# Kernel optimization log

Measured on AMD Instinct MI355X. Metric: run time of the kernel, lower is better.

Reference implementation:

```python
import jax, jax.numpy as jnp
import numpy as np

B, T, C = 2, 2048, 2048
H = 16
D = C // H  # 128 head dim
EPS = 1.1920929e-07  # torch RMSNorm default eps for fp32 (finfo.eps)
ROPE_BASE = 1000000.0


def setup_inputs() -> dict:
    key = jax.random.key(0)
    k1, k2, k3 = jax.random.split(key, 3)
    x = jax.random.normal(k1, (B, T, C), dtype=jnp.float32)
    w_qkv = jax.random.normal(k2, (C, 3 * C), dtype=jnp.float32) * (C ** -0.5)
    w_proj = jax.random.normal(k3, (C, C), dtype=jnp.float32) * (C ** -0.5)
    q_norm_w = jnp.ones((D,), dtype=jnp.float32)
    k_norm_w = jnp.ones((D,), dtype=jnp.float32)
    return {"x": x, "w_qkv": w_qkv, "w_proj": w_proj,
            "q_norm_w": q_norm_w, "k_norm_w": k_norm_w}


def _rms_norm(x, w):
    var = jnp.mean(jnp.square(x), axis=-1, keepdims=True)
    return x * jax.lax.rsqrt(var + EPS) * w


def _rope_tables(t_len, d_head, dtype):
    inv_freq = 1.0 / (ROPE_BASE ** (jnp.arange(0, d_head, 2, dtype=jnp.float32) / d_head))
    t = jnp.arange(t_len, dtype=jnp.float32)
    freqs = jnp.einsum('i,j->ij', t, inv_freq)          # [T, D/2]
    emb = jnp.concatenate([freqs, freqs], axis=-1)      # [T, D]
    return jnp.cos(emb).astype(dtype), jnp.sin(emb).astype(dtype)


def _rotate_half(x):
    x1, x2 = x[..., : x.shape[-1] // 2], x[..., x.shape[-1] // 2:]
    return jnp.concatenate([-x2, x1], axis=-1)


def reference(x, w_qkv, w_proj, q_norm_w, k_norm_w):
    b, t, c = x.shape
    qkv = x @ w_qkv                                     # [B, T, 3C]
    q, k, v = jnp.split(qkv, 3, axis=-1)
    # [B, H, T, D]
    q = q.reshape(b, t, H, D).transpose(0, 2, 1, 3)
    k = k.reshape(b, t, H, D).transpose(0, 2, 1, 3)
    v = v.reshape(b, t, H, D).transpose(0, 2, 1, 3)
    q = _rms_norm(q, q_norm_w)
    k = _rms_norm(k, k_norm_w)
    cos, sin = _rope_tables(t, D, x.dtype)              # [T, D]
    q = q * cos + _rotate_half(q) * sin
    k = k * cos + _rotate_half(k) * sin
    # NOTE: module uses scale = 1/d_head, not 1/sqrt(d_head)
    scale = 1.0 / D
    att = jnp.einsum('bhqd,bhkd->bhqk', q, k) * scale   # [B, H, T, T]
    causal = jnp.tril(jnp.ones((t, t), dtype=bool))
    att = jnp.where(causal, att, jnp.finfo(att.dtype).min)
    att = jax.nn.softmax(att, axis=-1)
    y = jnp.einsum('bhqk,bhkd->bhqd', att, v)           # [B, H, T, D]
    y = y.transpose(0, 2, 1, 3).reshape(b, t, c)
    return y @ w_proj
```

## Files before the change

### kernel.cpp

```cpp
#include <hip/hip_runtime.h>
#include <stdint.h>

#define Bb   2
#define Tt   2048
#define Cc_  2048
#define Hh   16
#define Dd   128
#define Mm_  4096
#define N1   6144
#define EPSf 1.1920929e-07f
#define SCALE (1.0f/128.0f)

typedef __bf16 bf16;
typedef __attribute__((ext_vector_type(8))) __bf16 bf16x8;
typedef __attribute__((ext_vector_type(4))) float  f32x4;

__device__ __forceinline__ void gl_lds16(const bf16* g, bf16* l) {
  __builtin_amdgcn_global_load_lds(
      (const __attribute__((address_space(1))) unsigned int*)g,
      (__attribute__((address_space(3))) unsigned int*)l, 16, 0, 0);
}

__global__ __launch_bounds__(256) void cvt_bf16(const float* __restrict__ in,
                                                bf16* __restrict__ out, int n) {
  int i = (blockIdx.x * 256 + threadIdx.x) * 4;
  if (i >= n) return;
  float4 v = *(const float4*)(in + i);
  union { bf16 h[4]; uint2 u; } o;
  o.h[0] = (bf16)v.x; o.h[1] = (bf16)v.y; o.h[2] = (bf16)v.z; o.h[3] = (bf16)v.w;
  *(uint2*)(out + i) = o.u;
}

__global__ __launch_bounds__(256) void transpose_cvt(const float* __restrict__ in,
                                                     bf16* __restrict__ out,
                                                     int R, int Cc) {
  __shared__ float tile[64][65];
  int c0 = blockIdx.x * 64, r0 = blockIdx.y * 64;
  int tid = threadIdx.x;
#pragma unroll
  for (int j = 0; j < 16; ++j) {
    int idx = tid + j * 256;
    int r = idx >> 6, c = idx & 63;
    tile[r][c] = in[(size_t)(r0 + r) * Cc + c0 + c];
  }
  __syncthreads();
#pragma unroll
  for (int j = 0; j < 16; ++j) {
    int idx = tid + j * 256;
    int rr = idx & 63, cc = idx >> 6;
    out[(size_t)(c0 + cc) * R + r0 + rr] = (bf16)tile[rr][cc];
  }
}

__global__ __launch_bounds__(256) void gemm_qkv_fused(
    const bf16* __restrict__ A, const bf16* __restrict__ Bt,
    const float* __restrict__ qw, const float* __restrict__ kw,
    bf16* __restrict__ Qg, bf16* __restrict__ Kg, bf16* __restrict__ VgT) {
  __shared__ __align__(16) bf16 smem[128 * 129];
  bf16* As = smem;
  bf16* Bs = smem + 128 * 64;
  const int Kk = Cc_;
  const int tid = threadIdx.x;
  const int wave = tid >> 6, lane = tid & 63;
  const int quad = lane >> 4, li = lane & 15;
  const int wm = wave >> 1, wn = wave & 1;
  const int m0 = blockIdx.y * 128, n0 = blockIdx.x * 128;

  f32x4 acc[4][4] = {};

  for (int kt = 0; kt < Kk; kt += 64) {
    __syncthreads();
#pragma unroll
    for (int j = 0; j < 4; ++j) {
      int c = j * 256 + tid;
      int r = c >> 3, cc = c & 7;
      int gc = ((cc ^ (r & 7)) << 3);
      gl_lds16(A + (size_t)(m0 + r) * Kk + kt + gc, &As[c * 8]);
      gl_lds16(Bt + (size_t)(n0 + r) * Kk + kt + gc, &Bs[c * 8]);
    }
    __syncthreads();
#pragma unroll
    for (int kc = 0; kc < 2; ++kc) {
      bf16x8 af[4], bfr[4];
#pragma unroll
      for (int t = 0; t < 4; ++t) {
        int rowa = wm * 64 + t * 16 + li;
        af[t] = *(const bf16x8*)&As[rowa * 64 + (((kc * 4 + quad) ^ (rowa & 7)) << 3)];
        int rowb = wn * 64 + t * 16 + li;
        bfr[t] = *(const bf16x8*)&Bs[rowb * 64 + (((kc * 4 + quad) ^ (rowb & 7)) << 3)];
      }
#pragma unroll
      for (int mi = 0; mi < 4; ++mi)
#pragma unroll
        for (int ni = 0; ni < 4; ++ni)
          acc[mi][ni] = __builtin_amdgcn_mfma_f32_16x16x32_bf16(af[mi], bfr[ni],
                                                                acc[mi][ni], 0, 0, 0);
    }
  }

  __syncthreads();
  bf16 (*tile)[129] = (bf16(*)[129])smem;
#pragma unroll
  for (int mi = 0; mi < 4; ++mi) {
    int row = wm * 64 + mi * 16 + quad * 4;
#pragma unroll
    for (int ni = 0; ni < 4; ++ni) {
      int col = wn * 64 + ni * 16 + li;
#pragma unroll
      for (int r = 0; r < 4; ++r)
        tile[row + r][col] = (bf16)acc[mi][ni][r];
    }
  }
  __syncthreads();

  const int s = blockIdx.x;
  const int b = m0 >> 11;
  const int tloc = m0 & 2047;

  if (s < 32) {
    const float* w = (s < 16) ? qw : kw;
    bf16* Og = (s < 16) ? Qg : Kg;
    const int h = s & 15;
    const float w1 = w[lane], w2 = w[lane + 64];
    const float invf = exp2f((float)lane * (-19.9315685693241740f / 64.0f));
    const size_t hb = (size_t)(b * Hh + h) * Tt;
    for (int rr = 0; rr < 32; ++rr) {
      int row = wave * 32 + rr;
      float x1 = (float)tile[row][lane], x2 = (float)tile[row][lane + 64];
      float ss = x1 * x1 + x2 * x2;
#pragma unroll
      for (int o = 1; o < 64; o <<= 1) ss += __shfl_xor(ss, o);
      float rn = rsqrtf(ss * (1.0f / 128.0f) + EPSf);
      x1 *= rn * w1; x2 *= rn * w2;
      int t = tloc + row;
      float sn, cs;
      sincosf((float)t * invf, &sn, &cs);
      size_t o1 = (hb + t) * Dd + lane;
      Og[o1]      = (bf16)(x1 * cs - x2 * sn);
      Og[o1 + 64] = (bf16)(x2 * cs + x1 * sn);
    }
  } else {
    const int h = s - 32;
    const size_t hb = (size_t)(b * Hh + h) * Dd;
#pragma unroll
    for (int it = 0; it < 8; ++it) {
      int d = it * 16 + (tid >> 4);
      int t0 = (tid & 15) * 8;
      bf16x8 v;
#pragma unroll
      for (int j = 0; j < 8; ++j) v[j] = tile[t0 + j][d];
      *(bf16x8*)(VgT + (hb + d) * Tt + tloc + t0) = v;
    }
  }
}

template <typename OutT>
__global__ __launch_bounds__(512, 2) void gemm256(const bf16* __restrict__ A,
                                                  const bf16* __restrict__ Bt,
                                                  OutT* __restrict__ Cm,
                                                  int Nn, int Kk) {
  __shared__ __align__(16) bf16 As[2][256 * 64];
  __shared__ __align__(16) bf16 Bs[2][128 * 64];
  const int tid = threadIdx.x;
  const int wave = tid >> 6, lane = tid & 63;
  const int quad = lane >> 4, li = lane & 15;
  const int wm = wave >> 2, wn = wave & 3;

  const int nwg = gridDim.x * gridDim.y;
  const int wg  = blockIdx.y * gridDim.x + blockIdx.x;
  const int swz = (wg & 7) * (nwg >> 3) + (wg >> 3);
  const int m0 = (swz / gridDim.x) * 256;
  const int n0 = (swz % gridDim.x) * 128;

  const int NT = Kk >> 6;
  const int lrow = lane >> 3;
  const int lchk = (lane & 7) ^ lrow;

  auto stageA = [&](int tt, int h, int cb) {
    int kt = (tt < NT ? tt : NT - 1) << 6;
#pragma unroll
    for (int j = 0; j < 2; ++j) {
      int seg = j * 8 + wave;
      int r0 = ((seg >> 3) << 7) + (h << 6) + ((seg & 7) << 3);
      gl_lds16(A + (size_t)(m0 + r0 + lrow) * Kk + kt + (lchk << 3),
               &As[cb][r0 * 64]);
    }
  };
  auto stageB = [&](int tt, int cb) {
    int kt = (tt < NT ? tt : NT - 1) << 6;
#pragma unroll
    for (int j = 0; j < 2; ++j) {
      int seg = j * 8 + wave;
      int r0 = seg << 3;
      gl_lds16(Bt + (size_t)(n0 + r0 + lrow) * Kk + kt + (lchk << 3),
               &Bs[cb][r0 * 64]);
    }
  };

  f32x4 acc[8][2] = {};
  bf16x8 afr[4][2], bfr[2][2];

  auto rdA = [&](int h, int cb) {
#pragma unroll
    for (int mi = 0; mi < 4; ++mi) {
      int r = wm * 128 + h * 64 + mi * 16 + li;
#pragma unroll
      for (int kc = 0; kc < 2; ++kc)
        afr[mi][kc] = *(const bf16x8*)&As[cb][r * 64 + (((kc * 4 + quad) ^ (r & 7)) << 3)];
    }
  };
  auto rdB = [&](int cb) {
#pragma unroll
    for (int nj = 0; nj < 2; ++nj) {
      int r = wn * 32 + nj * 16 + li;
#pragma unroll
      for (int kc = 0; kc < 2; ++kc)
        bfr[nj][kc] = *(const bf16x8*)&Bs[cb][r * 64 + (((kc * 4 + quad) ^ (r & 7)) << 3)];
    }
  };
  auto mmac = [&](int mo) {
    __builtin_amdgcn_s_setprio(1);
#pragma unroll
    for (int kc = 0; kc < 2; ++kc)
#pragma unroll
      for (int mi = 0; mi < 4; ++mi)
#pragma unroll
        for (int nj = 0; nj < 2; ++nj)
          acc[mo + mi][nj] = __builtin_amdgcn_mfma_f32_16x16x32_bf16(
              afr[mi][kc], bfr[nj][kc], acc[mo + mi][nj], 0, 0, 0);
    __builtin_amdgcn_s_setprio(0);
  };

  auto tile = [&](int t, int cur, int nxt) {
    rdA(0, cur); rdB(cur);
    stageA(t + 1, 1, nxt);
    asm volatile("s_waitcnt lgkmcnt(8)" ::: "memory");
    __builtin_amdgcn_s_barrier();
    asm volatile("s_waitcnt lgkmcnt(0)" ::: "memory");
    __builtin_amdgcn_sched_barrier(0);
    mmac(0);
    asm volatile("s_waitcnt vmcnt(6)" ::: "memory");
    __builtin_amdgcn_s_barrier();
    rdA(1, cur);
    stageA(t + 2, 0, cur);
    stageB(t + 2, cur);
    __builtin_amdgcn_s_barrier();
    asm volatile("s_waitcnt lgkmcnt(0)" ::: "memory");
    __builtin_amdgcn_sched_barrier(0);
    mmac(4);
    asm volatile("s_waitcnt vmcnt(6)" ::: "memory");
    __builtin_amdgcn_s_barrier();
  };

  stageA(0, 0, 0); stageB(0, 0); stageA(0, 1, 0);
  stageA(1, 0, 1); stageB(1, 1);
  asm volatile("s_waitcnt vmcnt(6)" ::: "memory");
  __builtin_amdgcn_s_barrier();

  for (int t = 0; t < NT; t += 2) {
    tile(t, 0, 1);
    tile(t + 1, 1, 0);
  }
  asm volatile("s_waitcnt vmcnt(0)" ::: "memory");

#pragma unroll
  for (int mi = 0; mi < 8; ++mi) {
    int row = m0 + wm * 128 + mi * 16 + quad * 4;
#pragma unroll
    for (int nj = 0; nj < 2; ++nj) {
      int col = n0 + wn * 32 + nj * 16 + li;
#pragma unroll
      for (int r = 0; r < 4; ++r)
        Cm[(size_t)(row + r) * Nn + col] = (OutT)acc[mi][nj][r];
    }
  }
}

__global__ __launch_bounds__(256, 3) void attn(const bf16* __restrict__ Qg,
                                               const bf16* __restrict__ Kg,
                                               const bf16* __restrict__ VgT,
                                               bf16* __restrict__ Yg) {
  __shared__ __align__(16) bf16 Kl[64 * 128];
  __shared__ __align__(16) bf16 Vl[128 * 64];
  __shared__ __align__(16) bf16 Pl[4 * 16 * 72];
  const int bh = blockIdx.x;
  const int qt = (int)gridDim.y - 1 - (int)blockIdx.y;
  const int b = bh >> 4, h = bh & 15;
  const int tid = threadIdx.x, wave = tid >> 6, lane = tid & 63;
  const int quad = lane >> 4, li = lane & 15;
  const int q0 = qt * 64;

  const bf16* Qbase = Qg + ((size_t)bh * Tt + q0 + wave * 16 + li) * Dd;
  bf16x8 qf[4];
#pragma unroll
  for (int kc = 0; kc < 4; ++kc) qf[kc] = *(const bf16x8*)(Qbase + kc * 32 + quad * 8);

  f32x4 o[8] = {};
  float L[4] = {};
  bf16* Pw = &Pl[wave * 16 * 72];

  bf16x8 kreg[4];
  auto loadK = [&](int k0) {
#pragma unroll
    for (int j = 0; j < 4; ++j) {
      int c = j * 256 + tid;
      int r = c >> 4, cc = c & 15;
      kreg[j] = *(const bf16x8*)(Kg + ((size_t)bh * Tt + k0 + r) * Dd + ((cc ^ (r & 7)) << 3));
    }
  };
  auto stageV = [&](int k0) {
#pragma unroll
    for (int j = 0; j < 4; ++j) {
      int c = j * 256 + tid;
      int r = c >> 3, cc = c & 7;
      gl_lds16(VgT + ((size_t)bh * Dd + r) * Tt + k0 + ((cc ^ (r & 7)) << 3), &Vl[c * 8]);
    }
  };

  loadK(0);
  stageV(0);

  for (int kt = 0; kt <= qt; ++kt) {
    asm volatile("s_waitcnt vmcnt(4)" ::: "memory");
#pragma unroll
    for (int j = 0; j < 4; ++j) {
      int c = j * 256 + tid;
      *(bf16x8*)&Kl[c * 8] = kreg[j];
    }
    if (kt < qt) loadK(kt * 64 + 64);
    asm volatile("s_waitcnt lgkmcnt(0)" ::: "memory");
    __builtin_amdgcn_s_barrier();
    __builtin_amdgcn_sched_barrier(0);

    f32x4 s4[4] = {};
#pragma unroll
    for (int nt = 0; nt < 4; ++nt) {
      int key = nt * 16 + li;
#pragma unroll
      for (int kc = 0; kc < 4; ++kc) {
        bf16x8 kf = *(const bf16x8*)&Kl[key * 128 + (((kc * 4 + quad) ^ (key & 7)) << 3)];
        s4[nt] = __builtin_amdgcn_mfma_f32_16x16x32_bf16(qf[kc], kf, s4[nt], 0, 0, 0);
      }
    }
    const bool diag = (kt == qt);
#pragma unroll
    for (int nt = 0; nt < 4; ++nt)
#pragma unroll
      for (int r = 0; r < 4; ++r) {
        float e = __expf(s4[nt][r] * SCALE);
        if (diag && (nt * 16 + li > wave * 16 + quad * 4 + r)) e = 0.f;
        L[r] += e;
        Pw[(quad * 4 + r) * 72 + nt * 16 + li] = (bf16)e;
      }
    if (kt < qt) { asm volatile("s_waitcnt vmcnt(4)" ::: "memory"); }
    else         { asm volatile("s_waitcnt vmcnt(0)" ::: "memory"); }
    __builtin_amdgcn_s_barrier();
    __builtin_amdgcn_sched_barrier(0);

#pragma unroll
    for (int kc = 0; kc < 2; ++kc) {
      bf16x8 pf = *(const bf16x8*)&Pw[li * 72 + kc * 32 + quad * 8];
#pragma unroll
      for (int u = 0; u < 8; ++u) {
        bf16x8 vf = *(const bf16x8*)&Vl[(u * 16 + li) * 64 + (((kc * 4 + quad) ^ (li & 7)) << 3)];
        o[u] = __builtin_amdgcn_mfma_f32_16x16x32_bf16(pf, vf, o[u], 0, 0, 0);
      }
    }
    asm volatile("" ::: "memory");
    __builtin_amdgcn_s_barrier();
    __builtin_amdgcn_sched_barrier(0);
    if (kt < qt) stageV(kt * 64 + 64);
  }

  float inv[4];
#pragma unroll
  for (int r = 0; r < 4; ++r) {
    float s0 = L[r];
#pragma unroll
    for (int off = 1; off < 16; off <<= 1) s0 += __shfl_xor(s0, off);
    inv[r] = 1.0f / s0;
  }
  int trow = q0 + wave * 16 + quad * 4;
#pragma unroll
  for (int u = 0; u < 8; ++u) {
    int col = h * Dd + u * 16 + li;
#pragma unroll
    for (int r = 0; r < 4; ++r)
      Yg[(size_t)(b * Tt + trow + r) * Cc_ + col] = (bf16)(o[u][r] * inv[r]);
  }
}

extern "C" void kernel_launch(void* const* d_in, const int* in_sizes, int n_in,
                              void* d_out, int out_size, void* d_ws, size_t ws_size,
                              hipStream_t stream) {
  const float* x      = (const float*)d_in[0];
  const float* w_qkv  = (const float*)d_in[1];
  const float* w_proj = (const float*)d_in[2];
  const float* qnw    = (const float*)d_in[3];
  const float* knw    = (const float*)d_in[4];
  float* out = (float*)d_out;

  bf16* xb     = (bf16*)d_ws;
  bf16* wqkvT  = xb + (size_t)Mm_ * Cc_;
  bf16* wprojT = wqkvT + (size_t)N1 * Cc_;
  bf16* Qg     = wprojT + (size_t)Cc_ * Cc_;
  bf16* Kg     = Qg + (size_t)Bb * Hh * Tt * Dd;
  bf16* VgT    = Kg + (size_t)Bb * Hh * Tt * Dd;
  bf16* Yg     = xb;

  hipLaunchKernelGGL(cvt_bf16, dim3((Mm_ * Cc_ / 4) / 256), dim3(256), 0, stream,
                     x, xb, Mm_ * Cc_);
  hipLaunchKernelGGL(transpose_cvt, dim3(N1 / 64, Cc_ / 64), dim3(256), 0, stream,
                     w_qkv, wqkvT, Cc_, N1);
  hipLaunchKernelGGL(transpose_cvt, dim3(Cc_ / 64, Cc_ / 64), dim3(256), 0, stream,
                     w_proj, wprojT, Cc_, Cc_);
  hipLaunchKernelGGL(gemm_qkv_fused, dim3(N1 / 128, Mm_ / 128), dim3(256), 0, stream,
                     xb, wqkvT, qnw, knw, Qg, Kg, VgT);
  hipLaunchKernelGGL(attn, dim3(Bb * Hh, Tt / 64), dim3(256), 0, stream,
                     Qg, Kg, VgT, Yg);
  hipLaunchKernelGGL(gemm256<float>, dim3(Cc_ / 128, Mm_ / 256), dim3(512), 0, stream,
                     Yg, wprojT, out, Cc_, Cc_);
}
```

Measured before the change: 392.2 us.

## Precompute RoPE table and vectorize QKV epilogue norm/rope and V transpose

Adds a small kernel that precomputes cos/sin RoPE tables into workspace, so the QKV GEMM epilogue loads them instead of calling sincosf per element. The Q/K epilogue is reworked to process 4 rows per wave iteration with vectorized bf16x4 LDS reads and global stores, using a 16-lane shuffle reduction. The V path writes the tile transposed into LDS so the output can be read as contiguous bf16x8 vectors. This adds an extra launch and a table read from global memory, and the transposed LDS writes may cause bank conflicts.

```diff
diff --git a/kernel.cpp b/kernel.cpp
--- a/kernel.cpp
+++ b/kernel.cpp
@@ -13,6 +13,7 @@
 
 typedef __bf16 bf16;
 typedef __attribute__((ext_vector_type(8))) __bf16 bf16x8;
+typedef __attribute__((ext_vector_type(4))) __bf16 bf16x4;
 typedef __attribute__((ext_vector_type(4))) float  f32x4;
 
 __device__ __forceinline__ void gl_lds16(const bf16* g, bf16* l) {
@@ -31,6 +32,15 @@
   *(uint2*)(out + i) = o.u;
 }
 
+__global__ __launch_bounds__(256) void rope_tab(float2* __restrict__ rope) {
+  int i = blockIdx.x * 256 + threadIdx.x;
+  int t = i >> 6, d = i & 63;
+  float ang = (float)t * exp2f((float)d * (-19.9315685693241740f / 64.0f));
+  float sn, cs;
+  sincosf(ang, &sn, &cs);
+  rope[i] = make_float2(cs, sn);
+}
+
 __global__ __launch_bounds__(256) void transpose_cvt(const float* __restrict__ in,
                                                      bf16* __restrict__ out,
                                                      int R, int Cc) {
@@ -55,8 +65,9 @@
 __global__ __launch_bounds__(256) void gemm_qkv_fused(
     const bf16* __restrict__ A, const bf16* __restrict__ Bt,
     const float* __restrict__ qw, const float* __restrict__ kw,
+    const float2* __restrict__ rope,
     bf16* __restrict__ Qg, bf16* __restrict__ Kg, bf16* __restrict__ VgT) {
-  __shared__ __align__(16) bf16 smem[128 * 129];
+  __shared__ __align__(16) bf16 smem[128 * 136];
   bf16* As = smem;
   bf16* Bs = smem + 128 * 64;
   const int Kk = Cc_;
@@ -99,56 +110,83 @@
   }
 
   __syncthreads();
-  bf16 (*tile)[129] = (bf16(*)[129])smem;
-#pragma unroll
-  for (int mi = 0; mi < 4; ++mi) {
-    int row = wm * 64 + mi * 16 + quad * 4;
-#pragma unroll
-    for (int ni = 0; ni < 4; ++ni) {
-      int col = wn * 64 + ni * 16 + li;
-#pragma unroll
-      for (int r = 0; r < 4; ++r)
-        tile[row + r][col] = (bf16)acc[mi][ni][r];
-    }
-  }
-  __syncthreads();
-
   const int s = blockIdx.x;
   const int b = m0 >> 11;
   const int tloc = m0 & 2047;
+  bf16 (*tile)[136] = (bf16(*)[136])smem;
 
   if (s < 32) {
+#pragma unroll
+    for (int mi = 0; mi < 4; ++mi) {
+      int row = wm * 64 + mi * 16 + quad * 4;
+#pragma unroll
+      for (int ni = 0; ni < 4; ++ni) {
+        int col = wn * 64 + ni * 16 + li;
+#pragma unroll
+        for (int r = 0; r < 4; ++r)
+          tile[row + r][col] = (bf16)acc[mi][ni][r];
+      }
+    }
+    __syncthreads();
+
     const float* w = (s < 16) ? qw : kw;
     bf16* Og = (s < 16) ? Qg : Kg;
     const int h = s & 15;
-    const float w1 = w[lane], w2 = w[lane + 64];
-    const float invf = exp2f((float)lane * (-19.9315685693241740f / 64.0f));
     const size_t hb = (size_t)(b * Hh + h) * Tt;
-    for (int rr = 0; rr < 32; ++rr) {
-      int row = wave * 32 + rr;
-      float x1 = (float)tile[row][lane], x2 = (float)tile[row][lane + 64];
-      float ss = x1 * x1 + x2 * x2;
-#pragma unroll
-      for (int o = 1; o < 64; o <<= 1) ss += __shfl_xor(ss, o);
+    float w1[4], w2[4];
+#pragma unroll
+    for (int j = 0; j < 4; ++j) { w1[j] = w[li * 4 + j]; w2[j] = w[64 + li * 4 + j]; }
+#pragma unroll
+    for (int it = 0; it < 8; ++it) {
+      int row = wave * 32 + it * 4 + quad;
+      int t = tloc + row;
+      bf16x4 x1 = *(const bf16x4*)&tile[row][li * 4];
+      bf16x4 x2 = *(const bf16x4*)&tile[row][64 + li * 4];
+      float f1[4], f2[4];
+      float ss = 0.f;
+#pragma unroll
+      for (int j = 0; j < 4; ++j) {
+        f1[j] = (float)x1[j]; f2[j] = (float)x2[j];
+        ss += f1[j] * f1[j] + f2[j] * f2[j];
+      }
+#pragma unroll
+      for (int o = 1; o < 16; o <<= 1) ss += __shfl_xor(ss, o);
       float rn = rsqrtf(ss * (1.0f / 128.0f) + EPSf);
-      x1 *= rn * w1; x2 *= rn * w2;
-      int t = tloc + row;
-      float sn, cs;
-      sincosf((float)t * invf, &sn, &cs);
-      size_t o1 = (hb + t) * Dd + lane;
-      Og[o1]      = (bf16)(x1 * cs - x2 * sn);
-      Og[o1 + 64] = (bf16)(x2 * cs + x1 * sn);
+      const float4* rp = (const float4*)(rope + t * 64 + li * 4);
+      float4 ra = rp[0], rb = rp[1];
+      float cs[4] = {ra.x, ra.z, rb.x, rb.z};
+      float sn[4] = {ra.y, ra.w, rb.y, rb.w};
+      bf16x4 o1, o2;
+#pragma unroll
+      for (int j = 0; j < 4; ++j) {
+        float a1 = f1[j] * rn * w1[j], a2 = f2[j] * rn * w2[j];
+        o1[j] = (bf16)(a1 * cs[j] - a2 * sn[j]);
+        o2[j] = (bf16)(a2 * cs[j] + a1 * sn[j]);
+      }
+      size_t ob = (hb + t) * Dd + li * 4;
+      *(bf16x4*)(Og + ob)      = o1;
+      *(bf16x4*)(Og + ob + 64) = o2;
     }
   } else {
+#pragma unroll
+    for (int mi = 0; mi < 4; ++mi) {
+      int row = wm * 64 + mi * 16 + quad * 4;
+#pragma unroll
+      for (int ni = 0; ni < 4; ++ni) {
+        int col = wn * 64 + ni * 16 + li;
+#pragma unroll
+        for (int r = 0; r < 4; ++r)
+          tile[col][row + r] = (bf16)acc[mi][ni][r];
+      }
+    }
+    __syncthreads();
     const int h = s - 32;
     const size_t hb = (size_t)(b * Hh + h) * Dd;
 #pragma unroll
     for (int it = 0; it < 8; ++it) {
-      int d = it * 16 + (tid >> 4);
+      int d  = it * 16 + (tid >> 4);
       int t0 = (tid & 15) * 8;
-      bf16x8 v;
-#pragma unroll
-      for (int j = 0; j < 8; ++j) v[j] = tile[t0 + j][d];
+      bf16x8 v = *(const bf16x8*)&tile[d][t0];
       *(bf16x8*)(VgT + (hb + d) * Tt + tloc + t0) = v;
     }
   }
@@ -406,8 +444,10 @@
   bf16* Qg     = wprojT + (size_t)Cc_ * Cc_;
   bf16* Kg     = Qg + (size_t)Bb * Hh * Tt * Dd;
   bf16* VgT    = Kg + (size_t)Bb * Hh * Tt * Dd;
+  float2* rope = (float2*)(VgT + (size_t)Bb * Hh * Tt * Dd);
   bf16* Yg     = xb;
 
+  hipLaunchKernelGGL(rope_tab, dim3(Tt * 64 / 256), dim3(256), 0, stream, rope);
   hipLaunchKernelGGL(cvt_bf16, dim3((Mm_ * Cc_ / 4) / 256), dim3(256), 0, stream,
                      x, xb, Mm_ * Cc_);
   hipLaunchKernelGGL(transpose_cvt, dim3(N1 / 64, Cc_ / 64), dim3(256), 0, stream,
@@ -415,7 +455,7 @@
   hipLaunchKernelGGL(transpose_cvt, dim3(Cc_ / 64, Cc_ / 64), dim3(256), 0, stream,
                      w_proj, wprojT, Cc_, Cc_);
   hipLaunchKernelGGL(gemm_qkv_fused, dim3(N1 / 128, Mm_ / 128), dim3(256), 0, stream,
-                     xb, wqkvT, qnw, knw, Qg, Kg, VgT);
+                     xb, wqkvT, qnw, knw, rope, Qg, Kg, VgT);
   hipLaunchKernelGGL(attn, dim3(Bb * Hh, Tt / 64), dim3(256), 0, stream,
                      Qg, Kg, VgT, Yg);
   hipLaunchKernelGGL(gemm256<float>, dim3(Cc_ / 128, Mm_ / 256), dim3(512), 0, stream,
```

Result: faster. 377.8 us (-3.7%).
